# Kernel optimization log

Hardware: AMD Instinct MI355X
Metric: run time of the kernel (lower is better)

## Reference

```python
import jax, jax.numpy as jnp
import numpy as np

DIM = 768
NUM_HEADS = 12
H_SCALE = 1000.0


def setup_inputs() -> dict:
    key = jax.random.key(0)
    ks = jax.random.split(key, 6)
    B, N, C = 4, 1024, DIM
    x = jax.random.normal(ks[0], (B, N, C), dtype=jnp.float32)
    # elevations in meters: uniform in [0, 3000)
    elevation_patches = jax.random.uniform(ks[1], (B, N), dtype=jnp.float32) * 3000.0
    # torch nn.Linear weights are [out_features, in_features]
    W_qkv = jax.random.normal(ks[2], (3 * C, C), dtype=jnp.float32) * (1.0 / np.sqrt(C))
    W_proj = jax.random.normal(ks[3], (C, C), dtype=jnp.float32) * (1.0 / np.sqrt(C))
    b_proj = jnp.zeros((C,), dtype=jnp.float32)
    alpha = jnp.asarray(1.0, dtype=jnp.float32)
    return {"x": x, "elevation_patches": elevation_patches, "W_qkv": W_qkv,
            "W_proj": W_proj, "b_proj": b_proj, "alpha": alpha}


def reference(x, elevation_patches, W_qkv, W_proj, b_proj, alpha):
    B, N, C = x.shape
    H = NUM_HEADS
    hd = C // H
    scale = hd ** -0.5
    # qkv projection (no bias): [B, N, 3C] -> [3, B, H, N, hd]
    qkv = (x @ W_qkv.T).reshape(B, N, 3, H, hd).transpose(2, 0, 3, 1, 4)
    q, k, v = qkv[0], qkv[1], qkv[2]
    # scores: [B, H, N, N]
    scores = jnp.einsum("bhid,bhjd->bhij", q, k) * scale
    # elevation bias: penalty for uphill attention (j higher than i)
    elev_diff = (elevation_patches[:, None, :] - elevation_patches[:, :, None]) / H_SCALE
    bias = jnp.clip(-alpha * jax.nn.relu(elev_diff), -10.0, 0.0)  # [B, N, N]
    scores = scores + bias[:, None, :, :]
    attn = jax.nn.softmax(scores, axis=-1)
    # output: [B, H, N, hd] -> [B, N, C]
    out = jnp.einsum("bhij,bhjd->bhid", attn, v).transpose(0, 2, 1, 3).reshape(B, N, C)
    return out @ W_proj.T + b_proj
```

## Files before the change

kernel.cpp:

```cpp
#include <hip/hip_runtime.h>
#include <stdint.h>

typedef _Float16 f16;
typedef __attribute__((ext_vector_type(8))) _Float16 half8;
typedef __attribute__((ext_vector_type(4))) _Float16 half4;
typedef __attribute__((ext_vector_type(4))) float f32x4;

#define BATCH   4
#define NSEQ    1024
#define DIMC    768
#define NHEADS  12
#define HDIM    64
#define CQKV    2304
#define MROWS   4096
#define LOG2E   1.4426950408889634f
#define SCLQ    (0.125f * LOG2E)
#define CLIP2   (10.0f * LOG2E)

__device__ __forceinline__ void gload_lds16(const void* g, void* l) {
    __builtin_amdgcn_global_load_lds(
        (const __attribute__((address_space(1))) void*)g,
        (__attribute__((address_space(3))) void*)l, 16, 0, 0);
}

__global__ void cvt3_kernel(const float* __restrict__ x, const float* __restrict__ wq,
                            const float* __restrict__ wp,
                            f16* __restrict__ xf, f16* __restrict__ wqf,
                            f16* __restrict__ wpf) {
    const int A0 = MROWS * DIMC / 4;
    const int A1 = A0 + CQKV * DIMC / 4;
    const int A2 = A1 + DIMC * DIMC / 4;
    int i = blockIdx.x * blockDim.x + threadIdx.x;
    if (i >= A2) return;
    const float* src; f16* dst; int j;
    if (i < A0)      { src = x;  dst = xf;  j = i; }
    else if (i < A1) { src = wq; dst = wqf; j = i - A0; }
    else             { src = wp; dst = wpf; j = i - A1; }
    float4 v = reinterpret_cast<const float4*>(src)[j];
    half4 h;
    h.x = (f16)v.x; h.y = (f16)v.y; h.z = (f16)v.z; h.w = (f16)v.w;
    reinterpret_cast<half4*>(dst)[j] = h;
}

template <int EPI, int BM, int BN>
__global__ __launch_bounds__(256, 4)
void gemm_f16(const f16* __restrict__ A, const f16* __restrict__ B, int Kdim,
              f16* __restrict__ qf, f16* __restrict__ kf, f16* __restrict__ vtf,
              float* __restrict__ outp, const float* __restrict__ bias) {
    constexpr int MF = BM / 32, NF = BN / 32;
    constexpr int CA = BM * 4, CB = BN * 4;
    constexpr int LPT = (BM + BN) / 64;
    __shared__ __align__(16) f16 lA[2][BM * 32];
    __shared__ __align__(16) f16 lB[2][BN * 32];
    const int tid = threadIdx.x;
    const int w = tid >> 6, lane = tid & 63;
    const int l15 = lane & 15, lg = lane >> 4;
    const int m0 = blockIdx.y * BM, n0 = blockIdx.x * BN;
    const int wm = w >> 1, wn = w & 1;

    auto stage = [&](int k0, int buf) {
#pragma unroll
        for (int r = 0; r < CA / 256; ++r) {
            int chunk = r * 256 + tid;
            int row = chunk >> 2, c8 = chunk & 3;
            int s = c8 ^ ((row >> 1) & 3);
            gload_lds16(A + (size_t)(m0 + row) * Kdim + k0 + s * 8,
                        &lA[buf][chunk * 8]);
        }
#pragma unroll
        for (int r = 0; r < CB / 256; ++r) {
            int chunk = r * 256 + tid;
            int row = chunk >> 2, c8 = chunk & 3;
            int s = c8 ^ ((row >> 1) & 3);
            gload_lds16(B + (size_t)(n0 + row) * Kdim + k0 + s * 8,
                        &lB[buf][chunk * 8]);
        }
    };

    f32x4 acc[MF][NF] = {};

    stage(0, 0);

    const int slotA = lg ^ ((l15 >> 1) & 3);
    const int nst = Kdim / 32;
    int cur = 0;
    for (int t = 0; t < nst; ++t) {
        if (t + 1 < nst) {
            stage((t + 1) * 32, cur ^ 1);
            if constexpr (LPT == 4)
                asm volatile("s_waitcnt vmcnt(4)" ::: "memory");
            else
                asm volatile("s_waitcnt vmcnt(2)" ::: "memory");
        } else {
            asm volatile("s_waitcnt vmcnt(0)" ::: "memory");
        }
        __builtin_amdgcn_s_barrier();
        __builtin_amdgcn_sched_barrier(0);

        half8 af[MF], bf[NF];
#pragma unroll
        for (int i = 0; i < MF; ++i) {
            int row = wm * (BM / 2) + i * 16 + l15;
            af[i] = *(const half8*)&lA[cur][row * 32 + slotA * 8];
        }
#pragma unroll
        for (int j = 0; j < NF; ++j) {
            int row = wn * (BN / 2) + j * 16 + l15;
            bf[j] = *(const half8*)&lB[cur][row * 32 + slotA * 8];
        }
#pragma unroll
        for (int m = 0; m < MF; ++m)
#pragma unroll
            for (int n = 0; n < NF; ++n)
                acc[m][n] = __builtin_amdgcn_mfma_f32_16x16x32_f16(af[m], bf[n], acc[m][n], 0, 0, 0);

        __builtin_amdgcn_sched_barrier(0);
        __builtin_amdgcn_s_barrier();
        cur ^= 1;
    }

    if constexpr (EPI == 0) {
#pragma unroll
        for (int n = 0; n < NF; ++n) {
            int col = n0 + wn * (BN / 2) + n * 16 + l15;
            int sec = col / 768;
            int rem = col - sec * 768;
            int hh = rem >> 6, dd = rem & 63;
#pragma unroll
            for (int m = 0; m < MF; ++m) {
                int rb = m0 + wm * (BM / 2) + m * 16 + 4 * lg;
                int b = rb >> 10, i0 = rb & 1023;
                if (sec == 0) {
#pragma unroll
                    for (int r = 0; r < 4; ++r)
                        qf[((size_t)(b * NHEADS + hh) * NSEQ + i0 + r) * HDIM + dd] =
                            (f16)(acc[m][n][r] * SCLQ);
                } else if (sec == 1) {
#pragma unroll
                    for (int r = 0; r < 4; ++r)
                        kf[((size_t)(b * NHEADS + hh) * NSEQ + i0 + r) * HDIM + dd] =
                            (f16)acc[m][n][r];
                } else {
                    half4 hv;
                    hv.x = (f16)acc[m][n][0]; hv.y = (f16)acc[m][n][1];
                    hv.z = (f16)acc[m][n][2]; hv.w = (f16)acc[m][n][3];
                    *(half4*)&vtf[((size_t)(b * NHEADS + hh) * HDIM + dd) * NSEQ + i0] = hv;
                }
            }
        }
    } else {
#pragma unroll
        for (int n = 0; n < NF; ++n) {
            int col = n0 + wn * (BN / 2) + n * 16 + l15;
            float bv = bias[col];
#pragma unroll
            for (int m = 0; m < MF; ++m) {
                int rb = m0 + wm * (BM / 2) + m * 16 + 4 * lg;
#pragma unroll
                for (int r = 0; r < 4; ++r)
                    outp[(size_t)(rb + r) * DIMC + col] = acc[m][n][r] + bv;
            }
        }
    }
}

__global__ __launch_bounds__(256, 3)
void attn_f16(const f16* __restrict__ qf, const f16* __restrict__ kf,
              const f16* __restrict__ vtf, const float* __restrict__ elev,
              const float* __restrict__ alphap, f16* __restrict__ aof) {
    __shared__ __align__(16) f16 lK[2][64 * 64];
    __shared__ __align__(16) f16 lV[2][64 * 64];
    __shared__ __align__(16) f16 lP[4][1024];
    __shared__ __align__(16) float lElev[NSEQ];
    const int tid = threadIdx.x;
    const int w = tid >> 6, lane = tid & 63;
    const int l15 = lane & 15, lg = lane >> 4;

    const int bid = blockIdx.x;
    const int lid = (bid & 7) * 96 + (bid >> 3);
    const int q0 = (lid & 15) * 64;
    const int bh = lid >> 4;
    const int b = bh / NHEADS, h = bh - b * NHEADS;
    const float esc = alphap[0] * (LOG2E * 0.001f);
    const size_t base = (size_t)bh * NSEQ * HDIM;
    const size_t vbase = (size_t)bh * HDIM * NSEQ;

    const int ch0 = tid, ch1 = 256 + tid;
    const int r0 = ch0 >> 3, s0 = ((ch0 & 7) ^ (r0 & 7)) * 8;
    const int r1 = ch1 >> 3, s1 = ((ch1 & 7) ^ (r1 & 7)) * 8;

    auto stageKV = [&](int j0, int buf) {
        gload_lds16(kf + base + (size_t)(j0 + r0) * HDIM + s0, &lK[buf][ch0 * 8]);
        gload_lds16(kf + base + (size_t)(j0 + r1) * HDIM + s1, &lK[buf][ch1 * 8]);
        gload_lds16(vtf + vbase + (size_t)r0 * NSEQ + j0 + s0, &lV[buf][ch0 * 8]);
        gload_lds16(vtf + vbase + (size_t)r1 * NSEQ + j0 + s1, &lV[buf][ch1 * 8]);
    };

    stageKV(0, 0);

    {
        float4 e4 = reinterpret_cast<const float4*>(elev + b * NSEQ)[tid];
        *reinterpret_cast<float4*>(&lElev[tid * 4]) = e4;
    }
    half8 qa[2];
    {
        int qrow = q0 + w * 16 + l15;
#pragma unroll
        for (int ks = 0; ks < 2; ++ks)
            qa[ks] = *(const half8*)&qf[base + (size_t)qrow * HDIM + ks * 32 + 8 * lg];
    }
    __syncthreads();

    float ei2[4];
#pragma unroll
    for (int r = 0; r < 4; ++r)
        ei2[r] = lElev[q0 + w * 16 + 4 * lg + r] * esc;

    float prs[4] = {0.f, 0.f, 0.f, 0.f};
    f32x4 o[4] = {};

    const int sswz = l15 & 7;
    int cur = 0;
    for (int j0 = 0; j0 < NSEQ; j0 += 64) {
        if (j0 + 64 < NSEQ) {
            stageKV(j0 + 64, cur ^ 1);
            asm volatile("s_waitcnt vmcnt(4)" ::: "memory");
        } else {
            asm volatile("s_waitcnt vmcnt(0)" ::: "memory");
        }
        __builtin_amdgcn_s_barrier();
        __builtin_amdgcn_sched_barrier(0);

        f32x4 s[4] = {};
        __builtin_amdgcn_s_setprio(1);
#pragma unroll
        for (int n = 0; n < 4; ++n)
#pragma unroll
            for (int ks = 0; ks < 2; ++ks) {
                int slot = (ks * 4 + lg) ^ sswz;
                half8 kb8 = *(const half8*)&lK[cur][(n * 16 + l15) * 64 + slot * 8];
                s[n] = __builtin_amdgcn_mfma_f32_16x16x32_f16(qa[ks], kb8, s[n], 0, 0, 0);
            }
        __builtin_amdgcn_s_setprio(0);

#pragma unroll
        for (int n = 0; n < 4; ++n) {
            float ej = lElev[j0 + n * 16 + l15];
#pragma unroll
            for (int r = 0; r < 4; ++r) {
                float d2 = fmaf(ej, esc, -ei2[r]);
                float p = __builtin_amdgcn_exp2f(
                    s[n][r] - fminf(fmaxf(d2, 0.f), CLIP2));
                prs[r] += p;
                int prow = 4 * lg + r;
                int idx = prow * 64 + ((2 * n + (l15 >> 3)) ^ (prow & 7)) * 8 + (l15 & 7);
                lP[w][idx] = (f16)p;
            }
        }

        __builtin_amdgcn_s_setprio(1);
#pragma unroll
        for (int ks = 0; ks < 2; ++ks) {
            half8 pa = *(const half8*)&lP[w][l15 * 64 + ((ks * 4 + lg) ^ sswz) * 8];
#pragma unroll
            for (int df = 0; df < 4; ++df) {
                int slot = (ks * 4 + lg) ^ sswz;
                half8 vb = *(const half8*)&lV[cur][(df * 16 + l15) * 64 + slot * 8];
                o[df] = __builtin_amdgcn_mfma_f32_16x16x32_f16(pa, vb, o[df], 0, 0, 0);
            }
        }
        __builtin_amdgcn_s_setprio(0);

        __builtin_amdgcn_sched_barrier(0);
        __builtin_amdgcn_s_barrier();
        cur ^= 1;
    }

#pragma unroll
    for (int r = 0; r < 4; ++r) {
        prs[r] += __shfl_xor(prs[r], 1);
        prs[r] += __shfl_xor(prs[r], 2);
        prs[r] += __shfl_xor(prs[r], 4);
        prs[r] += __shfl_xor(prs[r], 8);
    }

#pragma unroll
    for (int r = 0; r < 4; ++r) {
        float inv = 1.0f / prs[r];
        int row = q0 + w * 16 + 4 * lg + r;
        size_t ob = ((size_t)b * NSEQ + row) * DIMC + h * HDIM;
#pragma unroll
        for (int df = 0; df < 4; ++df)
            aof[ob + df * 16 + l15] = (f16)(o[df][r] * inv);
    }
}

extern "C" void kernel_launch(void* const* d_in, const int* in_sizes, int n_in,
                              void* d_out, int out_size, void* d_ws, size_t ws_size,
                              hipStream_t stream) {
    const float* x     = (const float*)d_in[0];
    const float* elev  = (const float*)d_in[1];
    const float* wqkv  = (const float*)d_in[2];
    const float* wproj = (const float*)d_in[3];
    const float* bproj = (const float*)d_in[4];
    const float* alpha = (const float*)d_in[5];
    float* out = (float*)d_out;

    char* ws = (char*)d_ws;
    size_t off = 0;
    auto alloc = [&](size_t elems) {
        void* p = ws + off;
        off += (elems * 2 + 255) & ~(size_t)255;
        return (f16*)p;
    };
    const size_t szXW  = (size_t)MROWS * DIMC;
    const size_t szWQ  = (size_t)CQKV * DIMC;
    const size_t szWP  = (size_t)DIMC * DIMC;
    const size_t szQKV = (size_t)BATCH * NHEADS * NSEQ * HDIM;

    f16* xf  = alloc(szXW);
    f16* wqf = alloc(szWQ);
    f16* wpf = alloc(szWP);
    f16* qf  = alloc(szQKV);
    f16* kf  = alloc(szQKV);
    f16* vtf = alloc(szQKV);
    f16* aof = xf;
    (void)ws_size; (void)in_sizes; (void)n_in; (void)out_size;

    const int n4 = (int)((szXW + szWQ + szWP) / 4);
    cvt3_kernel<<<(n4 + 255) / 256, 256, 0, stream>>>(x, wqkv, wproj, xf, wqf, wpf);

    gemm_f16<0, 64, 64><<<dim3(CQKV / 64, MROWS / 64), 256, 0, stream>>>(
        xf, wqf, DIMC, qf, kf, vtf, nullptr, nullptr);

    attn_f16<<<BATCH * NHEADS * (NSEQ / 64), 256, 0, stream>>>(
        qf, kf, vtf, elev, alpha, aof);

    gemm_f16<1, 64, 64><<<dim3(DIMC / 64, MROWS / 64), 256, 0, stream>>>(
        aof, wpf, DIMC, nullptr, nullptr, nullptr, out, bproj);
}
```

Measured before the change: 92.45 us.

## Fuse fp32-to-fp16 conversion into GEMM loads and drop separate convert kernel

Removes the standalone conversion kernel. The GEMMs now read fp32 x and weights directly, convert them in registers and write fp16 tiles to LDS, which saves one launch and a round trip through global memory. The QKV GEMM moves to 128x128 tiles with 3 waves per SIMD, and the attention loop's wait/barrier placement changes to a single vmcnt(0) wait at the end of each iteration. The cost is register-staged loads in place of direct-to-LDS loads, less overlap because the loop waits on vmcnt(0) every step, and weights reconverted by every block.

```diff
diff --git a/kernel.cpp b/kernel.cpp
--- a/kernel.cpp
+++ b/kernel.cpp
@@ -23,33 +23,20 @@
         (__attribute__((address_space(3))) void*)l, 16, 0, 0);
 }
 
-__global__ void cvt3_kernel(const float* __restrict__ x, const float* __restrict__ wq,
-                            const float* __restrict__ wp,
-                            f16* __restrict__ xf, f16* __restrict__ wqf,
-                            f16* __restrict__ wpf) {
-    const int A0 = MROWS * DIMC / 4;
-    const int A1 = A0 + CQKV * DIMC / 4;
-    const int A2 = A1 + DIMC * DIMC / 4;
-    int i = blockIdx.x * blockDim.x + threadIdx.x;
-    if (i >= A2) return;
-    const float* src; f16* dst; int j;
-    if (i < A0)      { src = x;  dst = xf;  j = i; }
-    else if (i < A1) { src = wq; dst = wqf; j = i - A0; }
-    else             { src = wp; dst = wpf; j = i - A1; }
-    float4 v = reinterpret_cast<const float4*>(src)[j];
-    half4 h;
-    h.x = (f16)v.x; h.y = (f16)v.y; h.z = (f16)v.z; h.w = (f16)v.w;
-    reinterpret_cast<half4*>(dst)[j] = h;
+__device__ __forceinline__ half8 cvt8(float4 u, float4 v) {
+    half8 h;
+    h[0] = (f16)u.x; h[1] = (f16)u.y; h[2] = (f16)u.z; h[3] = (f16)u.w;
+    h[4] = (f16)v.x; h[5] = (f16)v.y; h[6] = (f16)v.z; h[7] = (f16)v.w;
+    return h;
 }
 
 template <int EPI, int BM, int BN>
-__global__ __launch_bounds__(256, 4)
-void gemm_f16(const f16* __restrict__ A, const f16* __restrict__ B, int Kdim,
+__global__ __launch_bounds__(256, EPI == 0 ? 3 : 4)
+void gemm_f16(const void* Ap, const float* Bp, int Kdim,
               f16* __restrict__ qf, f16* __restrict__ kf, f16* __restrict__ vtf,
               float* __restrict__ outp, const float* __restrict__ bias) {
     constexpr int MF = BM / 32, NF = BN / 32;
-    constexpr int CA = BM * 4, CB = BN * 4;
-    constexpr int LPT = (BM + BN) / 64;
+    constexpr int PA = BM / 64, PB = BN / 64;
     __shared__ __align__(16) f16 lA[2][BM * 32];
     __shared__ __align__(16) f16 lB[2][BN * 32];
     const int tid = threadIdx.x;
@@ -58,44 +45,69 @@
     const int m0 = blockIdx.y * BM, n0 = blockIdx.x * BN;
     const int wm = w >> 1, wn = w & 1;
 
-    auto stage = [&](int k0, int buf) {
-#pragma unroll
-        for (int r = 0; r < CA / 256; ++r) {
-            int chunk = r * 256 + tid;
-            int row = chunk >> 2, c8 = chunk & 3;
-            int s = c8 ^ ((row >> 1) & 3);
-            gload_lds16(A + (size_t)(m0 + row) * Kdim + k0 + s * 8,
-                        &lA[buf][chunk * 8]);
-        }
-#pragma unroll
-        for (int r = 0; r < CB / 256; ++r) {
-            int chunk = r * 256 + tid;
-            int row = chunk >> 2, c8 = chunk & 3;
-            int s = c8 ^ ((row >> 1) & 3);
-            gload_lds16(B + (size_t)(n0 + row) * Kdim + k0 + s * 8,
-                        &lB[buf][chunk * 8]);
+    const float* Af32 = (const float*)Ap;
+    const f16*   Af16 = (const f16*)Ap;
+
+    float4 ra[PA][2], rb[PB][2];
+
+    auto loadA = [&](int k0, int buf) {
+        if constexpr (EPI == 0) {
+#pragma unroll
+            for (int p = 0; p < PA; ++p) {
+                int c = p * 256 + tid, row = c >> 2, sl = c & 3;
+                const float* s = Af32 + (size_t)(m0 + row) * Kdim + k0 + sl * 8;
+                ra[p][0] = *(const float4*)s;
+                ra[p][1] = *(const float4*)(s + 4);
+            }
+        } else {
+#pragma unroll
+            for (int p = 0; p < BM / 64; ++p) {
+                int c = p * 256 + tid, row = c >> 2, c8 = c & 3;
+                int s = c8 ^ ((row >> 1) & 3);
+                gload_lds16(Af16 + (size_t)(m0 + row) * Kdim + k0 + s * 8,
+                            &lA[buf][c * 8]);
+            }
+        }
+    };
+    auto loadB = [&](int k0) {
+#pragma unroll
+        for (int p = 0; p < PB; ++p) {
+            int c = p * 256 + tid, row = c >> 2, sl = c & 3;
+            const float* s = Bp + (size_t)(n0 + row) * Kdim + k0 + sl * 8;
+            rb[p][0] = *(const float4*)s;
+            rb[p][1] = *(const float4*)(s + 4);
+        }
+    };
+    auto writeAB = [&](int buf) {
+        if constexpr (EPI == 0) {
+#pragma unroll
+            for (int p = 0; p < PA; ++p) {
+                int c = p * 256 + tid, row = c >> 2, sl = c & 3;
+                int ph = sl ^ ((row >> 1) & 3);
+                *(half8*)&lA[buf][row * 32 + ph * 8] = cvt8(ra[p][0], ra[p][1]);
+            }
+        }
+#pragma unroll
+        for (int p = 0; p < PB; ++p) {
+            int c = p * 256 + tid, row = c >> 2, sl = c & 3;
+            int ph = sl ^ ((row >> 1) & 3);
+            *(half8*)&lB[buf][row * 32 + ph * 8] = cvt8(rb[p][0], rb[p][1]);
         }
     };
 
     f32x4 acc[MF][NF] = {};
 
-    stage(0, 0);
+    loadA(0, 0); loadB(0);
+    asm volatile("s_waitcnt vmcnt(0)" ::: "memory");
+    writeAB(0);
+    asm volatile("s_waitcnt lgkmcnt(0)" ::: "memory");
+    __builtin_amdgcn_s_barrier();
 
     const int slotA = lg ^ ((l15 >> 1) & 3);
     const int nst = Kdim / 32;
     int cur = 0;
     for (int t = 0; t < nst; ++t) {
-        if (t + 1 < nst) {
-            stage((t + 1) * 32, cur ^ 1);
-            if constexpr (LPT == 4)
-                asm volatile("s_waitcnt vmcnt(4)" ::: "memory");
-            else
-                asm volatile("s_waitcnt vmcnt(2)" ::: "memory");
-        } else {
-            asm volatile("s_waitcnt vmcnt(0)" ::: "memory");
-        }
-        __builtin_amdgcn_s_barrier();
-        __builtin_amdgcn_sched_barrier(0);
+        if (t + 1 < nst) { loadA((t + 1) * 32, cur ^ 1); loadB((t + 1) * 32); }
 
         half8 af[MF], bf[NF];
 #pragma unroll
@@ -114,7 +126,11 @@
             for (int n = 0; n < NF; ++n)
                 acc[m][n] = __builtin_amdgcn_mfma_f32_16x16x32_f16(af[m], bf[n], acc[m][n], 0, 0, 0);
 
-        __builtin_amdgcn_sched_barrier(0);
+        if (t + 1 < nst) {
+            asm volatile("s_waitcnt vmcnt(0)" ::: "memory");
+            writeAB(cur ^ 1);
+        }
+        asm volatile("s_waitcnt lgkmcnt(0)" ::: "memory");
         __builtin_amdgcn_s_barrier();
         cur ^= 1;
     }
@@ -128,8 +144,8 @@
             int hh = rem >> 6, dd = rem & 63;
 #pragma unroll
             for (int m = 0; m < MF; ++m) {
-                int rb = m0 + wm * (BM / 2) + m * 16 + 4 * lg;
-                int b = rb >> 10, i0 = rb & 1023;
+                int rb_ = m0 + wm * (BM / 2) + m * 16 + 4 * lg;
+                int b = rb_ >> 10, i0 = rb_ & 1023;
                 if (sec == 0) {
 #pragma unroll
                     for (int r = 0; r < 4; ++r)
@@ -155,10 +171,10 @@
             float bv = bias[col];
 #pragma unroll
             for (int m = 0; m < MF; ++m) {
-                int rb = m0 + wm * (BM / 2) + m * 16 + 4 * lg;
+                int rb_ = m0 + wm * (BM / 2) + m * 16 + 4 * lg;
 #pragma unroll
                 for (int r = 0; r < 4; ++r)
-                    outp[(size_t)(rb + r) * DIMC + col] = acc[m][n][r] + bv;
+                    outp[(size_t)(rb_ + r) * DIMC + col] = acc[m][n][r] + bv;
             }
         }
     }
@@ -222,14 +238,7 @@
     const int sswz = l15 & 7;
     int cur = 0;
     for (int j0 = 0; j0 < NSEQ; j0 += 64) {
-        if (j0 + 64 < NSEQ) {
-            stageKV(j0 + 64, cur ^ 1);
-            asm volatile("s_waitcnt vmcnt(4)" ::: "memory");
-        } else {
-            asm volatile("s_waitcnt vmcnt(0)" ::: "memory");
-        }
-        __builtin_amdgcn_s_barrier();
-        __builtin_amdgcn_sched_barrier(0);
+        if (j0 + 64 < NSEQ) stageKV(j0 + 64, cur ^ 1);
 
         f32x4 s[4] = {};
         __builtin_amdgcn_s_setprio(1);
@@ -271,7 +280,7 @@
         }
         __builtin_amdgcn_s_setprio(0);
 
-        __builtin_amdgcn_sched_barrier(0);
+        asm volatile("s_waitcnt vmcnt(0)" ::: "memory");
         __builtin_amdgcn_s_barrier();
         cur ^= 1;
     }
@@ -313,29 +322,20 @@
         off += (elems * 2 + 255) & ~(size_t)255;
         return (f16*)p;
     };
-    const size_t szXW  = (size_t)MROWS * DIMC;
-    const size_t szWQ  = (size_t)CQKV * DIMC;
-    const size_t szWP  = (size_t)DIMC * DIMC;
     const size_t szQKV = (size_t)BATCH * NHEADS * NSEQ * HDIM;
 
-    f16* xf  = alloc(szXW);
-    f16* wqf = alloc(szWQ);
-    f16* wpf = alloc(szWP);
     f16* qf  = alloc(szQKV);
     f16* kf  = alloc(szQKV);
     f16* vtf = alloc(szQKV);
-    f16* aof = xf;
+    f16* aof = alloc((size_t)MROWS * DIMC);
     (void)ws_size; (void)in_sizes; (void)n_in; (void)out_size;
 
-    const int n4 = (int)((szXW + szWQ + szWP) / 4);
-    cvt3_kernel<<<(n4 + 255) / 256, 256, 0, stream>>>(x, wqkv, wproj, xf, wqf, wpf);
-
-    gemm_f16<0, 64, 64><<<dim3(CQKV / 64, MROWS / 64), 256, 0, stream>>>(
-        xf, wqf, DIMC, qf, kf, vtf, nullptr, nullptr);
+    gemm_f16<0, 128, 128><<<dim3(CQKV / 128, MROWS / 128), 256, 0, stream>>>(
+        x, wqkv, DIMC, qf, kf, vtf, nullptr, nullptr);
 
     attn_f16<<<BATCH * NHEADS * (NSEQ / 64), 256, 0, stream>>>(
         qf, kf, vtf, elev, alpha, aof);
 
     gemm_f16<1, 64, 64><<<dim3(DIMC / 64, MROWS / 64), 256, 0, stream>>>(
-        aof, wpf, DIMC, nullptr, nullptr, nullptr, out, bproj);
-}
+        aof, wproj, DIMC, nullptr, nullptr, nullptr, out, bproj);
+}
```

After: 91.40 us. Within noise of the previous version (-1.1%).
